# Kernel tuning notes

Measured on AMD Instinct MI355X. Metric: run time of the kernel, lower is better.

The kernel has to match this reference:

```python
import jax, jax.numpy as jnp
import numpy as np

EPS = 1e-5
INV_SQRT2 = 0.7071067811865476

def _rmsnorm(x, w):
    rms = jnp.sqrt(jnp.sum(x * x, axis=-1) / x.shape[-1] + EPS)
    return x / rms[..., None] * w

def _gelu(x):
    # exact erf-based GELU as in the torch module
    return x * (1.0 + jax.scipy.special.erf(x * INV_SQRT2)) * 0.5

def setup_inputs() -> dict:
    key = jax.random.key(0)
    ks = jax.random.split(key, 8)
    B, S, D, DFF = 4, 2048, 1024, 4096
    s = 0.02  # realistic init scale keeps softmax non-degenerate
    return {
        "x": jax.random.normal(ks[0], (B, S, D), jnp.float32),
        "ln1": jax.random.uniform(ks[1], (D,), jnp.float32),
        "ln2": jax.random.uniform(ks[2], (D,), jnp.float32),
        "ffn1": jax.random.normal(ks[3], (DFF, D), jnp.float32) * s,
        "ffn2": jax.random.normal(ks[4], (D, DFF), jnp.float32) * s,
        "k_proj": jax.random.normal(ks[5], (D, D), jnp.float32) * s,
        "q_proj": jax.random.normal(ks[6], (D, D), jnp.float32) * s,
        "v_proj": jax.random.normal(ks[7], (D, D), jnp.float32) * s,
        "out_proj": jax.random.normal(jax.random.fold_in(key, 99), (D, D), jnp.float32) * s,
    }

def reference(x, ln1, ln2, ffn1, ffn2, k_proj, q_proj, v_proj, out_proj):
    S = x.shape[1]
    d_k = x.shape[-1]
    # --- attention branch (single-head, as in source) ---
    h = _rmsnorm(x, ln1)
    Q = h @ q_proj.T  # [B,S,D]
    K = h @ k_proj.T
    V = h @ v_proj.T
    scores = jnp.einsum('bqd,bkd->bqk', Q, K) / jnp.sqrt(jnp.float32(d_k))
    attn = jax.nn.softmax(scores, axis=-1)
    # source: softmax first, then zero out strict-upper (future) entries, renormalize
    causal = jnp.tril(jnp.ones((S, S), jnp.float32))
    attn = attn * causal
    attn = attn / jnp.sum(attn, axis=-1, keepdims=True)
    mh = jnp.einsum('bqk,bkd->bqd', attn, V) @ out_proj
    y = x + mh
    # --- FFN branch: NOTE source feeds RMSNorm2(x), not y ---
    h2 = _rmsnorm(x, ln2)
    ff = _gelu(h2 @ ffn1.T) @ ffn2.T
    return y + ff
```

## Files before the change

### kernel.cpp

```cpp
#include <hip/hip_runtime.h>
#include <math.h>

typedef __bf16 bf16_t;
typedef __bf16 bf16x8 __attribute__((ext_vector_type(8)));
typedef float f32x4 __attribute__((ext_vector_type(4)));

#define LDS16(g, l) __builtin_amdgcn_global_load_lds( \
    (__attribute__((address_space(1))) void*)(g),     \
    (__attribute__((address_space(3))) void*)(l), 16, 0, 0)

__global__ __launch_bounds__(256) void prep_kernel(
    const float* __restrict__ qp, const float* __restrict__ kp,
    const float* __restrict__ vp, const float* __restrict__ f1,
    const float* __restrict__ f2, const float* __restrict__ op,
    const float* __restrict__ x, const float* __restrict__ ln1,
    bf16_t* __restrict__ qkvb, bf16_t* __restrict__ f1b,
    bf16_t* __restrict__ f2b, bf16_t* __restrict__ opT,
    bf16_t* __restrict__ h1)
{
    __shared__ float tile[32][33];
    __shared__ float red[4];
    int bid = blockIdx.x;
    int t = threadIdx.x;
    if (bid < 11264) {
        size_t i = ((size_t)bid * 256 + t) * 4;
        const float* src;
        bf16_t* dst;
        if (i < 3145728) {
            if (i < 1048576)      { src = qp + i;             dst = qkvb + i; }
            else if (i < 2097152) { src = kp + (i - 1048576); dst = qkvb + i; }
            else                  { src = vp + (i - 2097152); dst = qkvb + i; }
        } else if (i < 7340032) { src = f1 + (i - 3145728); dst = f1b + (i - 3145728); }
        else                    { src = f2 + (i - 7340032); dst = f2b + (i - 7340032); }
        float4 v = *(const float4*)src;
        dst[0] = (bf16_t)v.x; dst[1] = (bf16_t)v.y;
        dst[2] = (bf16_t)v.z; dst[3] = (bf16_t)v.w;
    } else if (bid < 12288) {
        int b2 = bid - 11264;
        int c0 = (b2 & 31) * 32, r0 = (b2 >> 5) * 32;
        int tx = t & 31, ty = t >> 5;
#pragma unroll
        for (int i = 0; i < 32; i += 8)
            tile[ty + i][tx] = op[(size_t)(r0 + ty + i) * 1024 + c0 + tx];
        __syncthreads();
#pragma unroll
        for (int i = 0; i < 32; i += 8)
            opT[(size_t)(c0 + ty + i) * 1024 + r0 + tx] = (bf16_t)tile[tx][ty + i];
    } else {
        int row = bid - 12288;
        float4 xv = ((const float4*)(x + (size_t)row * 1024))[t];
        float ss = xv.x * xv.x + xv.y * xv.y + xv.z * xv.z + xv.w * xv.w;
#pragma unroll
        for (int o = 32; o > 0; o >>= 1) ss += __shfl_xor(ss, o, 64);
        if ((t & 63) == 0) red[t >> 6] = ss;
        __syncthreads();
        ss = red[0] + red[1] + red[2] + red[3];
        float rinv = rsqrtf(ss * (1.0f / 1024.0f) + 1e-5f);
        float4 wv = ((const float4*)ln1)[t];
        bf16_t* hp = h1 + (size_t)row * 1024 + t * 4;
        hp[0] = (bf16_t)(xv.x * rinv * wv.x);
        hp[1] = (bf16_t)(xv.y * rinv * wv.y);
        hp[2] = (bf16_t)(xv.z * rinv * wv.z);
        hp[3] = (bf16_t)(xv.w * rinv * wv.w);
    }
}

__global__ __launch_bounds__(256) void rmsnorm_kernel(
    const float* __restrict__ x, const float* __restrict__ w,
    bf16_t* __restrict__ h)
{
    int row = blockIdx.x;
    int t = threadIdx.x;
    float4 xv = ((const float4*)(x + (size_t)row * 1024))[t];
    float ss = xv.x * xv.x + xv.y * xv.y + xv.z * xv.z + xv.w * xv.w;
#pragma unroll
    for (int o = 32; o > 0; o >>= 1) ss += __shfl_xor(ss, o, 64);
    __shared__ float red[4];
    if ((t & 63) == 0) red[t >> 6] = ss;
    __syncthreads();
    ss = red[0] + red[1] + red[2] + red[3];
    float rinv = rsqrtf(ss * (1.0f / 1024.0f) + 1e-5f);
    float4 wv = ((const float4*)w)[t];
    bf16_t* hp = h + (size_t)row * 1024 + t * 4;
    hp[0] = (bf16_t)(xv.x * rinv * wv.x);
    hp[1] = (bf16_t)(xv.y * rinv * wv.y);
    hp[2] = (bf16_t)(xv.z * rinv * wv.z);
    hp[3] = (bf16_t)(xv.w * rinv * wv.w);
}

__global__ __launch_bounds__(256) void transpose_bf16(
    const bf16_t* __restrict__ in, bf16_t* __restrict__ out,
    int rows, int ldin, long long sIn, long long sOut)
{
    __shared__ bf16_t tile[32][33];
    int b = blockIdx.z;
    const bf16_t* ip = in + (long long)b * sIn;
    bf16_t* op = out + (long long)b * sOut;
    int c0 = blockIdx.x * 32, r0 = blockIdx.y * 32;
    int tx = threadIdx.x & 31, ty = threadIdx.x >> 5;
#pragma unroll
    for (int i = 0; i < 32; i += 8)
        tile[ty + i][tx] = ip[(size_t)(r0 + ty + i) * ldin + c0 + tx];
    __syncthreads();
#pragma unroll
    for (int i = 0; i < 32; i += 8)
        op[(size_t)(c0 + ty + i) * rows + r0 + tx] = tile[tx][ty + i];
}

__global__ __launch_bounds__(256) void causal_softmax_kernel(bf16_t* __restrict__ SP)
{
    const int S = 2048;
    int q = blockIdx.x, b = blockIdx.y;
    bf16_t* row = SP + ((size_t)b * S + q) * S;
    int t = threadIdx.x;
    int j0 = t * 8;
    int Jstore = ((q >> 7) + 1) << 7;

    float v[8];
    if (j0 + 7 <= q) {
        bf16x8 xv = *(const bf16x8*)(row + j0);
#pragma unroll
        for (int i = 0; i < 8; i++) v[i] = (float)xv[i];
    } else if (j0 <= q) {
#pragma unroll
        for (int i = 0; i < 8; i++)
            v[i] = (j0 + i <= q) ? (float)row[j0 + i] : -1e30f;
    } else {
#pragma unroll
        for (int i = 0; i < 8; i++) v[i] = -1e30f;
    }

    float mx = v[0];
#pragma unroll
    for (int i = 1; i < 8; i++) mx = fmaxf(mx, v[i]);
#pragma unroll
    for (int o = 32; o > 0; o >>= 1) mx = fmaxf(mx, __shfl_xor(mx, o, 64));
    __shared__ float sm[4], ssum[4];
    if ((t & 63) == 0) sm[t >> 6] = mx;
    __syncthreads();
    mx = fmaxf(fmaxf(sm[0], sm[1]), fmaxf(sm[2], sm[3]));

    float e[8];
    float sum = 0.f;
#pragma unroll
    for (int i = 0; i < 8; i++) {
        e[i] = (v[i] > -1e29f) ? expf(v[i] - mx) : 0.f;
        sum += e[i];
    }
#pragma unroll
    for (int o = 32; o > 0; o >>= 1) sum += __shfl_xor(sum, o, 64);
    if ((t & 63) == 0) ssum[t >> 6] = sum;
    __syncthreads();
    sum = ssum[0] + ssum[1] + ssum[2] + ssum[3];
    float r = 1.0f / sum;

    if (j0 < Jstore) {
        bf16x8 ov;
#pragma unroll
        for (int i = 0; i < 8; i++) ov[i] = (bf16_t)(e[i] * r);
        *(bf16x8*)(row + j0) = ov;
    }
}

template <int EPI, bool CSKIP, bool CKLOOP, bool ASPLIT>
__global__ __launch_bounds__(256) void gemm_bt(
    const bf16_t* __restrict__ A, const bf16_t* __restrict__ A2, int lda,
    const bf16_t* __restrict__ B, int ldb,
    void* Cv, int ldc, const float* R,
    int K, int Ksp, int Mt, long long sA, long long sB, long long sC,
    float scale)
{
    int id = blockIdx.x, bz = blockIdx.z;
    int xcd = id & 7, p = id >> 3;
    int chunk = Mt >> 3;
    int bm = xcd * chunk + (p % chunk);
    int bn = p / chunk;
    if (CSKIP && bn > bm) return;

    __shared__ __align__(16) bf16_t At[128 * 64];
    __shared__ __align__(16) bf16_t Bt[128 * 64];
    int t = threadIdx.x;
    int w = t >> 6, l = t & 63;
    int wm = w >> 1, wn = w & 1;
    int lane_m = l & 15, quad = l >> 4;

    const bf16_t* Ag = A + (long long)bz * sA + (size_t)(bm * 128) * lda;
    const bf16_t* Bg = B + (long long)bz * sB + (size_t)(bn * 128) * ldb;

    int Keff = K;
    if (CKLOOP) {
        int kk = (bm + 1) * 128;
        if (kk < K) Keff = kk;
    }

    f32x4 acc[4][4] = {};

    int rb = w * 8 + (l >> 3);
    int g0 = ((l & 7) ^ ((l >> 3) & 7)) * 8;
    const bf16_t* a0[4];
    const bf16_t* a1[4];
    const bf16_t* b0[4];
#pragma unroll
    for (int j = 0; j < 4; j++) {
        size_t ro = (size_t)(rb + 32 * j);
        a0[j] = Ag + ro * lda + g0;
        if (ASPLIT) a1[j] = A2 + (long long)bz * sA + (size_t)(bm * 128) * lda
                           + ro * lda + g0;
        b0[j] = Bg + ro * ldb + g0;
    }

    int s0 = (quad ^ (lane_m & 7)) * 8;
    int s1 = ((4 + quad) ^ (lane_m & 7)) * 8;

    for (int kt = 0; kt < Keff; kt += 64) {
        __syncthreads();
#pragma unroll
        for (int j = 0; j < 4; j++) {
            const bf16_t* pa = a0[j] + kt;
            if (ASPLIT && kt >= Ksp) pa = a1[j] + (kt - Ksp);
            LDS16(pa, At + (size_t)w * 512 + j * 2048);
            LDS16(b0[j] + kt, Bt + (size_t)w * 512 + j * 2048);
        }
        __syncthreads();

#pragma unroll
        for (int h = 0; h < 2; h++) {
            int sh = h ? s1 : s0;
            bf16x8 af[4], bfr[4];
#pragma unroll
            for (int mi = 0; mi < 4; mi++)
                af[mi] = *(const bf16x8*)(At + (wm * 64 + mi * 16 + lane_m) * 64 + sh);
#pragma unroll
            for (int ni = 0; ni < 4; ni++)
                bfr[ni] = *(const bf16x8*)(Bt + (wn * 64 + ni * 16 + lane_m) * 64 + sh);
#pragma unroll
            for (int mi = 0; mi < 4; mi++)
#pragma unroll
                for (int ni = 0; ni < 4; ni++)
                    acc[mi][ni] = __builtin_amdgcn_mfma_f32_16x16x32_bf16(
                        af[mi], bfr[ni], acc[mi][ni], 0, 0, 0);
        }
    }

    long long cbase = (long long)bz * sC;
#pragma unroll
    for (int mi = 0; mi < 4; mi++) {
#pragma unroll
        for (int r = 0; r < 4; r++) {
            int row = bm * 128 + wm * 64 + mi * 16 + quad * 4 + r;
#pragma unroll
            for (int ni = 0; ni < 4; ni++) {
                int col = bn * 128 + wn * 64 + ni * 16 + lane_m;
                float v = acc[mi][ni][r];
                size_t idx = (size_t)(cbase + (long long)row * ldc + col);
                if (EPI == 0) {
                    ((bf16_t*)Cv)[idx] = (bf16_t)(v * scale);
                } else if (EPI == 1) {
                    float g = 0.5f * v * (1.0f + erff(v * 0.70710678118654752f));
                    ((bf16_t*)Cv)[idx] = (bf16_t)g;
                } else {
                    float rv = R[(size_t)row * ldc + col];
                    ((float*)Cv)[idx] = v + rv;
                }
            }
        }
    }
}

#define VM8 asm volatile("s_waitcnt vmcnt(8)" ::: "memory")
#define VM4 asm volatile("s_waitcnt vmcnt(4)" ::: "memory")
#define VM0 asm volatile("s_waitcnt vmcnt(0)" ::: "memory")
#define NOP ((void)0)

#define STAGE_A(BUF, KH, KOFF) do { \
    LDS16(rA0 + (KOFF), &As[BUF][KH][w * 512]);        \
    LDS16(rA1 + (KOFF), &As[BUF][KH][4096 + w * 512]); } while (0)
#define STAGE_B(BUF, KH, KOFF) do { \
    LDS16(rB0 + (KOFF), &Bs[BUF][KH][w * 512]);        \
    LDS16(rB1 + (KOFF), &Bs[BUF][KH][4096 + w * 512]); } while (0)

#define PHASE(BUF, KH, MQ, STAGE_STMT, WAIT_STMT)                             \
  {                                                                           \
    _Pragma("unroll") for (int mi = 0; mi < 4; mi++)                          \
        af[mi] = *(const bf16x8*)&As[BUF][KH][arow + (MQ)*2048 + mi*512];     \
    if ((MQ) == 0) {                                                          \
      _Pragma("unroll") for (int ni = 0; ni < 4; ni++)                        \
          bfr[ni] = *(const bf16x8*)&Bs[BUF][KH][brow + ni*512];              \
    }                                                                         \
    STAGE_STMT;                                                               \
    __builtin_amdgcn_s_barrier();                                             \
    asm volatile("s_waitcnt lgkmcnt(0)" ::: "memory");                        \
    __builtin_amdgcn_sched_barrier(0);                                        \
    __builtin_amdgcn_s_setprio(1);                                            \
    _Pragma("unroll") for (int mi = 0; mi < 4; mi++)                          \
      _Pragma("unroll") for (int ni = 0; ni < 4; ni++)                        \
        acc[(MQ)*4 + mi][ni] = __builtin_amdgcn_mfma_f32_16x16x32_bf16(       \
            af[mi], bfr[ni], acc[(MQ)*4 + mi][ni], 0, 0, 0);                  \
    __builtin_amdgcn_s_setprio(0);                                            \
    WAIT_STMT;                                                                \
    __builtin_amdgcn_s_barrier();                                             \
  }

template <int EPI>
__global__ __launch_bounds__(512, 2) void gemm256(
    const bf16_t* __restrict__ A, int lda,
    const bf16_t* __restrict__ B, int ldb,
    void* Cv, int ldc, const float* R, int K, int Nt, float scale)
{
    int id = blockIdx.x;
    int xcd = id & 7, p = id >> 3;
    int chunk = gridDim.x >> 3;
    int g = xcd * chunk + p;
    int bm = g / Nt, bn = g % Nt;

    __shared__ __align__(16) bf16_t As[2][2][256 * 32];
    __shared__ __align__(16) bf16_t Bs[2][2][256 * 32];

    int t = threadIdx.x;
    int w = t >> 6, l = t & 63;
    int wm = w >> 2, wn = w & 3;
    int lm = l & 15, quad = l >> 4;

    const bf16_t* Ag = A + (size_t)(bm * 256) * lda;
    const bf16_t* Bg = B + (size_t)(bn * 256) * ldb;

    int g4 = ((l & 3) ^ ((l >> 2) & 3)) * 8;
    const bf16_t* rA0 = Ag + (size_t)(w * 16 + (l >> 2)) * lda + g4;
    const bf16_t* rA1 = rA0 + (size_t)128 * lda;
    const bf16_t* rB0 = Bg + (size_t)(w * 16 + (l >> 2)) * ldb + g4;
    const bf16_t* rB1 = rB0 + (size_t)128 * ldb;

    int slot8 = (quad ^ (lm & 3)) * 8;
    int arow = (wm * 128 + lm) * 32 + slot8;
    int brow = (wn * 64 + lm) * 32 + slot8;

    f32x4 acc[8][4] = {};
    bf16x8 af[4], bfr[4];

    STAGE_A(0, 0, 0);  STAGE_B(0, 0, 0);
    STAGE_A(0, 1, 32); STAGE_B(0, 1, 32);
    STAGE_A(1, 0, 64); STAGE_B(1, 0, 64);
    VM8;
    __builtin_amdgcn_s_barrier();

    int T = K >> 7;
    for (int it = 0; it < T - 1; ++it) {
        int kb = it << 7;
        PHASE(0, 0, 0, STAGE_A(1, 1, kb + 96),  NOP);
        PHASE(0, 0, 1, STAGE_B(1, 1, kb + 96),  VM8);
        PHASE(0, 1, 0, STAGE_A(0, 0, kb + 128), NOP);
        PHASE(0, 1, 1, STAGE_B(0, 0, kb + 128), VM8);
        PHASE(1, 0, 0, STAGE_A(0, 1, kb + 160), NOP);
        PHASE(1, 0, 1, STAGE_B(0, 1, kb + 160), VM8);
        PHASE(1, 1, 0, STAGE_A(1, 0, kb + 192), NOP);
        PHASE(1, 1, 1, STAGE_B(1, 0, kb + 192), VM8);
    }
    {
        int kb = (T - 1) << 7;
        PHASE(0, 0, 0, STAGE_A(1, 1, kb + 96), NOP);
        PHASE(0, 0, 1, STAGE_B(1, 1, kb + 96), VM8);
        PHASE(0, 1, 0, NOP, NOP);
        PHASE(0, 1, 1, NOP, VM4);
        PHASE(1, 0, 0, NOP, NOP);
        PHASE(1, 0, 1, NOP, VM0);
        PHASE(1, 1, 0, NOP, NOP);
        PHASE(1, 1, 1, NOP, NOP);
    }

#pragma unroll
    for (int mq = 0; mq < 2; mq++) {
#pragma unroll
        for (int mi = 0; mi < 4; mi++) {
#pragma unroll
            for (int r = 0; r < 4; r++) {
                int row = bm * 256 + wm * 128 + mq * 64 + mi * 16 + quad * 4 + r;
#pragma unroll
                for (int ni = 0; ni < 4; ni++) {
                    int col = bn * 256 + wn * 64 + ni * 16 + lm;
                    float v = acc[mq * 4 + mi][ni][r];
                    size_t idx = (size_t)row * ldc + col;
                    if (EPI == 0) {
                        ((bf16_t*)Cv)[idx] = (bf16_t)(v * scale);
                    } else if (EPI == 1) {
                        float ge = 0.5f * v * (1.0f + erff(v * 0.70710678118654752f));
                        ((bf16_t*)Cv)[idx] = (bf16_t)ge;
                    } else {
                        float rv = R[(size_t)row * ldc + col];
                        ((float*)Cv)[idx] = v + rv;
                    }
                }
            }
        }
    }
}

extern "C" void kernel_launch(void* const* d_in, const int* in_sizes, int n_in,
                              void* d_out, int out_size, void* d_ws, size_t ws_size,
                              hipStream_t stream)
{
    (void)in_sizes; (void)n_in; (void)out_size;
    const float* x    = (const float*)d_in[0];
    const float* ln1  = (const float*)d_in[1];
    const float* ln2  = (const float*)d_in[2];
    const float* ffn1 = (const float*)d_in[3];
    const float* ffn2 = (const float*)d_in[4];
    const float* kp   = (const float*)d_in[5];
    const float* qp   = (const float*)d_in[6];
    const float* vp   = (const float*)d_in[7];
    const float* op   = (const float*)d_in[8];
    float* out = (float*)d_out;

    const size_t MiB = 1048576;
    char* ws = (char*)d_ws;
    bf16_t* qkvb = (bf16_t*)(ws + 0 * MiB);
    bf16_t* opT  = (bf16_t*)(ws + 6 * MiB);
    bf16_t* f1b  = (bf16_t*)(ws + 8 * MiB);
    bf16_t* f2b  = (bf16_t*)(ws + 16 * MiB);
    bf16_t* h1   = (bf16_t*)(ws + 24 * MiB);
    bf16_t* VT   = (bf16_t*)(ws + 24 * MiB);
    bf16_t* h2   = (bf16_t*)(ws + 24 * MiB);
    bf16_t* QKVb = (bf16_t*)(ws + 40 * MiB);
    bf16_t* AV   = (bf16_t*)(ws + 40 * MiB);
    bf16_t* G0   = (bf16_t*)(ws + 40 * MiB);
    bf16_t* SP   = (bf16_t*)d_out;
    bool bigws = ws_size >= 104 * MiB;

    dim3 blk(256);
    dim3 blk5(512);
    const int HUGE_K = 1 << 30;

    prep_kernel<<<dim3(20480), blk, 0, stream>>>(
        qp, kp, vp, ffn1, ffn2, op, x, ln1, qkvb, f1b, f2b, opT, h1);

    gemm256<0><<<dim3(384), blk5, 0, stream>>>(
        h1, 1024, qkvb, 1024, QKVb, 3072, nullptr, 1024, 12, 1.0f);

    gemm_bt<0, true, false, false><<<dim3(256, 1, 4), blk, 0, stream>>>(
        QKVb, QKVb, 3072, QKVb + 1024, 3072, SP, 2048, nullptr,
        1024, HUGE_K, 16,
        (long long)2048 * 3072, (long long)2048 * 3072, (long long)2048 * 2048,
        1.0f / 32.0f);

    transpose_bf16<<<dim3(32, 64, 4), blk, 0, stream>>>(
        QKVb + 2048, VT, 2048, 3072,
        (long long)2048 * 3072, (long long)1024 * 2048);

    causal_softmax_kernel<<<dim3(2048, 4), blk, 0, stream>>>(SP);

    gemm_bt<0, false, true, false><<<dim3(128, 1, 4), blk, 0, stream>>>(
        SP, SP, 2048, VT, 2048, AV, 1024, nullptr,
        2048, HUGE_K, 16,
        (long long)2048 * 2048, (long long)1024 * 2048, (long long)2048 * 1024,
        1.0f);

    gemm256<2><<<dim3(128), blk5, 0, stream>>>(
        AV, 1024, opT, 1024, out, 1024, x, 1024, 4, 1.0f);

    rmsnorm_kernel<<<dim3(8192), blk, 0, stream>>>(x, ln2, h2);

    if (bigws) {
        gemm256<1><<<dim3(512), blk5, 0, stream>>>(
            h2, 1024, f1b, 1024, G0, 4096, nullptr, 1024, 16, 1.0f);
        gemm256<2><<<dim3(128), blk5, 0, stream>>>(
            G0, 4096, f2b, 4096, out, 1024, out, 4096, 4, 1.0f);
    } else {
        for (int half = 0; half < 2; half++) {
            gemm_bt<1, false, false, false><<<dim3(1024), blk, 0, stream>>>(
                h2, h2, 1024, f1b + (size_t)half * 2048 * 1024, 1024, G0, 2048,
                nullptr, 1024, HUGE_K, 64, 0, 0, 0, 1.0f);
            gemm_bt<2, false, false, false><<<dim3(512), blk, 0, stream>>>(
                G0, G0, 2048, f2b + half * 2048, 4096, out, 1024, out,
                2048, HUGE_K, 64, 0, 0, 0, 1.0f);
        }
    }
}
```

Measured before the change: 595.2 us.

## Split-K the FFN down-projection GEMM and change LDS swizzle pattern

The FFN2 GEMM (M=8192, N=1024, K=4096) previously launched only 128 blocks of 256x256 tiles, under-filling the GPU. It now splits K in two with a 2D grid of 256 blocks: the first half adds the residual and writes to out, the second writes a float partial to a workspace buffer, and a separate elementwise kernel sums them. The LDS XOR swizzle for the global-to-LDS loads and fragment reads also changes to use different lane bits, presumably to reduce bank conflicts. The split path runs only when the workspace is at least 136 MiB, and it costs an extra 32 MiB partial write and read plus one more kernel launch.

Result: faster. 554.2 us (-6.9%).

```diff
diff --git a/kernel.cpp b/kernel.cpp
--- a/kernel.cpp
+++ b/kernel.cpp
@@ -162,6 +162,19 @@
     }
 }
 
+__global__ __launch_bounds__(256) void addp_kernel(
+    float* __restrict__ out, const float* __restrict__ p1, int n4)
+{
+    int i = blockIdx.x * 256 + threadIdx.x;
+    int stride = gridDim.x * 256;
+    for (; i < n4; i += stride) {
+        float4 a = ((const float4*)out)[i];
+        float4 b = ((const float4*)p1)[i];
+        a.x += b.x; a.y += b.y; a.z += b.z; a.w += b.w;
+        ((float4*)out)[i] = a;
+    }
+}
+
 template <int EPI, bool CSKIP, bool CKLOOP, bool ASPLIT>
 __global__ __launch_bounds__(256) void gemm_bt(
     const bf16_t* __restrict__ A, const bf16_t* __restrict__ A2, int lda,
@@ -305,13 +318,15 @@
 __global__ __launch_bounds__(512, 2) void gemm256(
     const bf16_t* __restrict__ A, int lda,
     const bf16_t* __restrict__ B, int ldb,
-    void* Cv, int ldc, const float* R, int K, int Nt, float scale)
+    void* Cv, int ldc, const float* R, float* C2, int Ksp,
+    int K, int Nt, float scale)
 {
     int id = blockIdx.x;
     int xcd = id & 7, p = id >> 3;
     int chunk = gridDim.x >> 3;
     int g = xcd * chunk + p;
     int bm = g / Nt, bn = g % Nt;
+    int sK = (EPI == 3) ? blockIdx.y : 0;
 
     __shared__ __align__(16) bf16_t As[2][2][256 * 32];
     __shared__ __align__(16) bf16_t Bs[2][2][256 * 32];
@@ -321,16 +336,16 @@
     int wm = w >> 2, wn = w & 3;
     int lm = l & 15, quad = l >> 4;
 
-    const bf16_t* Ag = A + (size_t)(bm * 256) * lda;
-    const bf16_t* Bg = B + (size_t)(bn * 256) * ldb;
-
-    int g4 = ((l & 3) ^ ((l >> 2) & 3)) * 8;
+    const bf16_t* Ag = A + (size_t)(bm * 256) * lda + (size_t)sK * Ksp;
+    const bf16_t* Bg = B + (size_t)(bn * 256) * ldb + (size_t)sK * Ksp;
+
+    int g4 = ((l & 3) ^ ((l >> 3) & 3)) * 8;
     const bf16_t* rA0 = Ag + (size_t)(w * 16 + (l >> 2)) * lda + g4;
     const bf16_t* rA1 = rA0 + (size_t)128 * lda;
     const bf16_t* rB0 = Bg + (size_t)(w * 16 + (l >> 2)) * ldb + g4;
     const bf16_t* rB1 = rB0 + (size_t)128 * ldb;
 
-    int slot8 = (quad ^ (lm & 3)) * 8;
+    int slot8 = (quad ^ ((lm >> 1) & 3)) * 8;
     int arow = (wm * 128 + lm) * 32 + slot8;
     int brow = (wn * 64 + lm) * 32 + slot8;
 
@@ -384,9 +399,16 @@
                     } else if (EPI == 1) {
                         float ge = 0.5f * v * (1.0f + erff(v * 0.70710678118654752f));
                         ((bf16_t*)Cv)[idx] = (bf16_t)ge;
-                    } else {
+                    } else if (EPI == 2) {
                         float rv = R[(size_t)row * ldc + col];
                         ((float*)Cv)[idx] = v + rv;
+                    } else {
+                        if (sK == 0) {
+                            float rv = R[(size_t)row * ldc + col];
+                            ((float*)Cv)[idx] = v + rv;
+                        } else {
+                            C2[idx] = v;
+                        }
                     }
                 }
             }
@@ -422,8 +444,10 @@
     bf16_t* QKVb = (bf16_t*)(ws + 40 * MiB);
     bf16_t* AV   = (bf16_t*)(ws + 40 * MiB);
     bf16_t* G0   = (bf16_t*)(ws + 40 * MiB);
+    float*  P1   = (float*)(ws + 104 * MiB);
     bf16_t* SP   = (bf16_t*)d_out;
-    bool bigws = ws_size >= 104 * MiB;
+    bool bigws  = ws_size >= 104 * MiB;
+    bool splitw = ws_size >= 136 * MiB;
 
     dim3 blk(256);
     dim3 blk5(512);
@@ -433,7 +457,7 @@
         qp, kp, vp, ffn1, ffn2, op, x, ln1, qkvb, f1b, f2b, opT, h1);
 
     gemm256<0><<<dim3(384), blk5, 0, stream>>>(
-        h1, 1024, qkvb, 1024, QKVb, 3072, nullptr, 1024, 12, 1.0f);
+        h1, 1024, qkvb, 1024, QKVb, 3072, nullptr, nullptr, 0, 1024, 12, 1.0f);
 
     gemm_bt<0, true, false, false><<<dim3(256, 1, 4), blk, 0, stream>>>(
         QKVb, QKVb, 3072, QKVb + 1024, 3072, SP, 2048, nullptr,
@@ -454,15 +478,21 @@
         1.0f);
 
     gemm256<2><<<dim3(128), blk5, 0, stream>>>(
-        AV, 1024, opT, 1024, out, 1024, x, 1024, 4, 1.0f);
+        AV, 1024, opT, 1024, out, 1024, x, nullptr, 0, 1024, 4, 1.0f);
 
     rmsnorm_kernel<<<dim3(8192), blk, 0, stream>>>(x, ln2, h2);
 
     if (bigws) {
         gemm256<1><<<dim3(512), blk5, 0, stream>>>(
-            h2, 1024, f1b, 1024, G0, 4096, nullptr, 1024, 16, 1.0f);
-        gemm256<2><<<dim3(128), blk5, 0, stream>>>(
-            G0, 4096, f2b, 4096, out, 1024, out, 4096, 4, 1.0f);
+            h2, 1024, f1b, 1024, G0, 4096, nullptr, nullptr, 0, 1024, 16, 1.0f);
+        if (splitw) {
+            gemm256<3><<<dim3(128, 2), blk5, 0, stream>>>(
+                G0, 4096, f2b, 4096, out, 1024, out, P1, 2048, 2048, 4, 1.0f);
+            addp_kernel<<<dim3(2048), blk, 0, stream>>>(out, P1, 2097152);
+        } else {
+            gemm256<2><<<dim3(128), blk5, 0, stream>>>(
+                G0, 4096, f2b, 4096, out, 1024, out, nullptr, 0, 4096, 4, 1.0f);
+        }
     } else {
         for (int half = 0; half < 2; half++) {
             gemm_bt<1, false, false, false><<<dim3(1024), blk, 0, stream>>>(
```
